# Kernel tuning notes

Measured on AMD Instinct MI355X. Metric: run time of the kernel, lower is better.

## Reference

```python
import jax, jax.numpy as jnp
import numpy as np

B, S, D_MODEL, D_EMB, H = 2, 2048, 1024, 1024, 16
D_K = D_EMB // H


def setup_inputs() -> dict:
    key = jax.random.key(0)
    ks = jax.random.split(key, 14)
    sd_in = 1.0 / np.sqrt(D_MODEL)
    sd_e = 1.0 / np.sqrt(D_EMB)
    inp = {
        'q': jax.random.normal(ks[0], (B, S, D_MODEL), jnp.float32),
        'k': jax.random.normal(ks[1], (B, S, D_MODEL), jnp.float32),
        'v': jax.random.normal(ks[2], (B, S, D_MODEL), jnp.float32),
        # causal mask: 1 = attend, 0 = blocked (built from ones via tril)
        'mask': jnp.tril(jnp.ones((S, S), jnp.int32))[None].repeat(B, axis=0),
        # weights stored [in, out] (equivalent to torch Linear weight.T)
        'W_in': jax.random.uniform(ks[3], (D_MODEL, D_EMB), jnp.float32, -sd_in, sd_in),
        'b_in': jax.random.uniform(ks[4], (D_EMB,), jnp.float32, -sd_in, sd_in),
        'Wq': jax.random.uniform(ks[5], (D_EMB, D_EMB), jnp.float32, -sd_e, sd_e),
        'bq': jax.random.uniform(ks[6], (D_EMB,), jnp.float32, -sd_e, sd_e),
        'Wk': jax.random.uniform(ks[7], (D_EMB, D_EMB), jnp.float32, -sd_e, sd_e),
        'bk': jax.random.uniform(ks[8], (D_EMB,), jnp.float32, -sd_e, sd_e),
        'Wv': jax.random.uniform(ks[9], (D_EMB, D_EMB), jnp.float32, -sd_e, sd_e),
        'bv': jax.random.uniform(ks[10], (D_EMB,), jnp.float32, -sd_e, sd_e),
        'Wo': jax.random.uniform(ks[11], (D_EMB, D_MODEL), jnp.float32, -sd_e, sd_e),
        'bo': jax.random.uniform(ks[12], (D_MODEL,), jnp.float32, -sd_e, sd_e),
    }
    return inp


def reference(q, k, v, mask, W_in, b_in, Wq, bq, Wk, bk, Wv, bv, Wo, bo):
    bs = q.shape[0]
    # shared input projection applied to q, k, v (as in the torch module)
    q_p = q @ W_in + b_in
    k_p = k @ W_in + b_in
    v_p = v @ W_in + b_in
    # per-head projections -> [B, H, S, d_k]
    def heads(x):
        return x.reshape(bs, -1, H, D_K).transpose(0, 2, 1, 3)
    qh = heads(q_p @ Wq + bq)
    kh = heads(k_p @ Wk + bk)
    vh = heads(v_p @ Wv + bv)
    scores = jnp.einsum('bhqd,bhkd->bhqk', qh, kh) / np.sqrt(D_K).astype(np.float32)
    scores = jnp.where(mask[:, None, :, :] == 0, jnp.float32(-1e9), scores)
    attn = jax.nn.softmax(scores, axis=-1)  # dropout in eval mode = identity
    out_h = jnp.einsum('bhqk,bhkd->bhqd', attn, vh)
    concat = out_h.transpose(0, 2, 1, 3).reshape(bs, -1, D_EMB)
    return concat @ Wo + bo
```

## Files before the change

### kernel.cpp

```cpp
#include <hip/hip_runtime.h>
#include <hip/hip_bf16.h>
#include <stdint.h>

typedef __bf16 bf16;
typedef __bf16 bf16x4 __attribute__((ext_vector_type(4)));
typedef __bf16 bf16x8 __attribute__((ext_vector_type(8)));
typedef float  f32x4 __attribute__((ext_vector_type(4)));

#define MFMA16(a,b,c) __builtin_amdgcn_mfma_f32_16x16x32_bf16((a),(b),(c),0,0,0)

__device__ __forceinline__ void gld_lds16(const void* g, void* lds_base) {
  __builtin_amdgcn_global_load_lds(
      (const __attribute__((address_space(1))) unsigned int*)g,
      (__attribute__((address_space(3))) unsigned int*)(unsigned int)(uintptr_t)lds_base,
      16, 0, 0);
}

struct Cast4 { const float* src[4]; bf16* dst[4]; int nblk[4]; };
__global__ __launch_bounds__(256) void cast_bf16_k4(Cast4 c) {
  const int z = blockIdx.y;
  if ((int)blockIdx.x >= c.nblk[z]) return;
  const float* __restrict__ x = c.src[z];
  bf16* __restrict__ y = c.dst[z];
  size_t i = ((size_t)blockIdx.x * 256 + threadIdx.x) * 8;
  float4 a = *(const float4*)(x + i);
  float4 b = *(const float4*)(x + i + 4);
  bf16x8 o;
  o[0] = (bf16)a.x; o[1] = (bf16)a.y; o[2] = (bf16)a.z; o[3] = (bf16)a.w;
  o[4] = (bf16)b.x; o[5] = (bf16)b.y; o[6] = (bf16)b.z; o[7] = (bf16)b.w;
  *(bf16x8*)(y + i) = o;
}

struct TC4 { const float* src[4]; bf16* dst[4]; };
__global__ __launch_bounds__(256) void transpose_cast4(TC4 t) {
  __shared__ float tile[32][33];
  const float* __restrict__ W = t.src[blockIdx.z];
  bf16* __restrict__ Wt = t.dst[blockIdx.z];
  const int kbase = blockIdx.y * 32, nbase = blockIdx.x * 32;
  const int tx = threadIdx.x & 31, ty = threadIdx.x >> 5;
#pragma unroll
  for (int i = 0; i < 4; ++i)
    tile[ty + 8 * i][tx] = W[(size_t)(kbase + ty + 8 * i) * 1024 + nbase + tx];
  __syncthreads();
#pragma unroll
  for (int i = 0; i < 4; ++i)
    Wt[(size_t)(nbase + ty + 8 * i) * 1024 + kbase + tx] = (bf16)tile[tx][ty + 8 * i];
}

__global__ __launch_bounds__(256) void bias_combine(
    const float* __restrict__ b_in,
    const float* __restrict__ W0, const float* __restrict__ W1, const float* __restrict__ W2,
    const float* __restrict__ a0, const float* __restrict__ a1, const float* __restrict__ a2,
    float* __restrict__ outbase) {
  __shared__ float red[4][64];
  const int z = blockIdx.y;
  const float* W = z == 0 ? W0 : (z == 1 ? W1 : W2);
  const float* ba = z == 0 ? a0 : (z == 1 ? a1 : a2);
  const int tj = threadIdx.x & 63, ti = threadIdx.x >> 6;
  const int j = blockIdx.x * 64 + tj;
  float s = 0.f;
#pragma unroll 16
  for (int i = ti * 256; i < ti * 256 + 256; ++i) s += b_in[i] * W[(size_t)i * 1024 + j];
  red[ti][tj] = s;
  __syncthreads();
  if (ti == 0)
    outbase[z * 1024 + j] = ba[j] + red[0][tj] + red[1][tj] + red[2][tj] + red[3][tj];
}

struct Gemm3 {
  const bf16* A[3];
  const bf16* Bt[3];
  const float* bias[3];
  void* C[3];
  int vtz;
  bf16* Cvt;
};

template <bool OUT_BF16, int BN>
__global__ __launch_bounds__(256) void gemm_bt(Gemm3 g, int M, int N, int K) {
  constexpr int NB = BN / 32;
  const int nx = N / BN, nyl = (M >> 7) >> 3;
  const int bx = blockIdx.x;
  const int xcd = bx & 7;
  const int ib = bx >> 3;
  const int z = ib / (nx * nyl);
  const int r = ib - z * (nx * nyl);
  const int x = r / nyl;
  const int yl = r - x * nyl;
  const int y = xcd * nyl + yl;

  const bf16* __restrict__ A  = g.A[z];
  const bf16* __restrict__ Bt = g.Bt[z];
  const float* bias = g.bias[z];
  void* C = g.C[z];

  __shared__ bf16 As[128 * 64];
  __shared__ bf16 Bs[BN * 64];

  const int tid = threadIdx.x;
  const int lane = tid & 63;
  const int w = tid >> 6;
  const int wr = w >> 1, wc = w & 1;
  const int l16 = lane & 15, kg = lane >> 4;
  const int m0 = y * 128, n0 = x * BN;

  f32x4 acc[4][NB] = {};

  for (int k0 = 0; k0 < K; k0 += 64) {
#pragma unroll
    for (int i = 0; i < 4; ++i) {
      const int gc = i * 256 + tid;
      const int row = gc >> 3, ch = gc & 7;
      const int lch = ch ^ (row & 7);
      gld_lds16(A + (size_t)(m0 + row) * K + k0 + lch * 8,
                (char*)As + i * 4096 + w * 1024);
    }
#pragma unroll
    for (int i = 0; i < NB; ++i) {
      const int gc = i * 256 + tid;
      const int row = gc >> 3, ch = gc & 7;
      const int lch = ch ^ (row & 7);
      gld_lds16(Bt + (size_t)(n0 + row) * K + k0 + lch * 8,
                (char*)Bs + i * 4096 + w * 1024);
    }
    __syncthreads();
#pragma unroll
    for (int kk = 0; kk < 2; ++kk) {
      const int cc = kk * 4 + kg;
      bf16x8 af[4], bfr[NB];
#pragma unroll
      for (int m = 0; m < 4; ++m) {
        const int rr = wr * 64 + m * 16 + l16;
        af[m] = *(const bf16x8*)((const char*)As + rr * 128 + ((cc ^ (rr & 7)) << 4));
      }
#pragma unroll
      for (int n = 0; n < NB; ++n) {
        const int rn = wc * (BN / 2) + n * 16 + l16;
        bfr[n] = *(const bf16x8*)((const char*)Bs + rn * 128 + ((cc ^ (rn & 7)) << 4));
      }
#pragma unroll
      for (int m = 0; m < 4; ++m)
#pragma unroll
        for (int n = 0; n < NB; ++n)
          acc[m][n] = MFMA16(af[m], bfr[n], acc[m][n]);
    }
    __syncthreads();
  }

  if (z == g.vtz) {
#pragma unroll
    for (int m = 0; m < 4; ++m) {
      const int row0 = m0 + wr * 64 + m * 16 + kg * 4;
#pragma unroll
      for (int n = 0; n < NB; ++n) {
        const int col = n0 + wc * (BN / 2) + n * 16 + l16;
        const float bb = bias ? bias[col] : 0.f;
        bf16x4 pk;
#pragma unroll
        for (int i = 0; i < 4; ++i) pk[i] = (bf16)(acc[m][n][i] + bb);
        *(bf16x4*)(g.Cvt + (size_t)col * M + row0) = pk;
      }
    }
    return;
  }

#pragma unroll
  for (int m = 0; m < 4; ++m) {
    const int row0 = m0 + wr * 64 + m * 16 + kg * 4;
#pragma unroll
    for (int n = 0; n < NB; ++n) {
      const int col = n0 + wc * (BN / 2) + n * 16 + l16;
      const float bb = bias ? bias[col] : 0.f;
#pragma unroll
      for (int i = 0; i < 4; ++i) {
        float val = acc[m][n][i] + bb;
        if (OUT_BF16) ((bf16*)C)[(size_t)(row0 + i) * N + col] = (bf16)val;
        else          ((float*)C)[(size_t)(row0 + i) * N + col] = val;
      }
    }
  }
}

#define SEQL 2048
__global__ __launch_bounds__(512) void attn_flash(const bf16* __restrict__ qh,
                                                  const bf16* __restrict__ kh,
                                                  const bf16* __restrict__ vt,
                                                  bf16* __restrict__ conc) {
  const int bx = blockIdx.x;
  const int xcd = bx & 7, j = bx >> 3;
  const int half = j >> 5, jj = j & 31;
  const int bh = xcd * 4 + (jj >> 3);
  const int tq = jj & 7;
  const int rb = half ? tq : 15 - tq;
  const int b = bh >> 4, h = bh & 15;
  const int tid = threadIdx.x, lane = tid & 63, w = tid >> 6;
  const int wh = w >> 2;
  const int l16 = lane & 15, kg = lane >> 4;

  __shared__ bf16 KsB[2 * 8192];
  __shared__ bf16 VsB[2 * 8192];
  __shared__ bf16 Ps[8 * 1024];

  char* Psw = (char*)Ps + w * 2048;
  const size_t kvbase = ((size_t)(b * SEQL)) * 1024 + h * 64;
  const bf16* vbase = vt + ((size_t)(h * 64)) * 4096 + b * SEQL;

  auto stage = [&](int buf, int p) {
    const int j0 = p * 128;
#pragma unroll
    for (int c = 0; c < 2; ++c) {
      const int idx = c * 512 + tid;
      const int kr = idx >> 3;
      const int kch = (idx & 7) ^ (kr & 7);
      gld_lds16(kh + kvbase + (size_t)(j0 + kr) * 1024 + kch * 8,
                (char*)KsB + buf * 16384 + c * 8192 + w * 1024);
      const int vr = idx >> 4;
      const int vch = (idx & 15) ^ (vr & 15);
      gld_lds16(vbase + (size_t)vr * 4096 + j0 + vch * 8,
                (char*)VsB + buf * 16384 + c * 8192 + w * 1024);
    }
  };

  bf16x8 onesv;
#pragma unroll
  for (int i = 0; i < 8; ++i) onesv[i] = (bf16)1.0f;

  const int q0a = rb * 128;
  const int npairs = rb + 1;
  const int myrow0 = q0a + wh * 64 + (w & 3) * 16;
  const int rowmax = q0a + wh * 64 + 63;

  const int qrow = myrow0 + l16;
  const size_t qoff = ((size_t)(b * SEQL) + qrow) * 1024 + h * 64;
  const bf16x8 qf0 = *(const bf16x8*)(qh + qoff + kg * 8);
  const bf16x8 qf1 = *(const bf16x8*)(qh + qoff + 32 + kg * 8);

  f32x4 acc[4] = {};
  f32x4 accl = {};
  constexpr float SCL = 0.18033688011112042f;

  stage(0, 0);
  __syncthreads();

  for (int p = 0; p < npairs; ++p) {
    const int cur = p & 1;
    if (p + 1 < npairs) stage(cur ^ 1, p + 1);

    const char* Kb = (const char*)KsB + cur * 16384;
    const char* Vb = (const char*)VsB + cur * 16384;

#pragma unroll
    for (int s = 0; s < 2; ++s) {
      const int j0 = p * 128 + s * 64;
      if (j0 > rowmax) continue;

      f32x4 sc[4];
      __builtin_amdgcn_s_setprio(1);
#pragma unroll
      for (int kb = 0; kb < 4; ++kb) {
        const int r = s * 64 + kb * 16 + l16;
        bf16x8 kf0 = *(const bf16x8*)(Kb + r * 128 + ((kg ^ (r & 7)) << 4));
        bf16x8 kf1 = *(const bf16x8*)(Kb + r * 128 + (((4 + kg) ^ (r & 7)) << 4));
        f32x4 cfr = {};
        cfr = MFMA16(qf0, kf0, cfr);
        sc[kb] = MFMA16(qf1, kf1, cfr);
      }
      __builtin_amdgcn_s_setprio(0);

      if (j0 + 63 > myrow0) {
#pragma unroll
        for (int kb = 0; kb < 4; ++kb) {
          const int key = j0 + kb * 16 + l16;
#pragma unroll
          for (int i = 0; i < 4; ++i) {
            const int row = myrow0 + kg * 4 + i;
            if (key > row) sc[kb][i] = -1e9f;
          }
        }
      }
#pragma unroll
      for (int kb = 0; kb < 4; ++kb)
#pragma unroll
        for (int i = 0; i < 4; ++i) {
          const float pp2 = __builtin_exp2f(sc[kb][i] * SCL);
          const int prr = kg * 4 + i;
          const int ce = kb * 16 + l16;
          *(bf16*)(Psw + prr * 128 + ((((ce >> 3) ^ (prr & 7)) << 4) | ((ce & 7) * 2))) =
              (bf16)pp2;
        }

      __builtin_amdgcn_s_setprio(1);
#pragma unroll
      for (int kc = 0; kc < 2; ++kc) {
        bf16x8 pf = *(const bf16x8*)(Psw + l16 * 128 + ((((kc * 4 + kg) ^ (l16 & 7)) << 4)));
        accl = MFMA16(pf, onesv, accl);
#pragma unroll
        for (int nb = 0; nb < 4; ++nb) {
          const int rr = nb * 16 + l16;
          const int c16 = s * 8 + kc * 4 + kg;
          bf16x8 vf = *(const bf16x8*)(Vb + rr * 256 + ((c16 ^ (rr & 15)) << 4));
          acc[nb] = MFMA16(pf, vf, acc[nb]);
        }
      }
      __builtin_amdgcn_s_setprio(0);
    }
    __syncthreads();
  }

#pragma unroll
  for (int nb = 0; nb < 4; ++nb)
#pragma unroll
    for (int i = 0; i < 4; ++i) {
      const float val = acc[nb][i] / accl[i];
      const int row = myrow0 + kg * 4 + i;
      conc[((size_t)(b * SEQL) + row) * 1024 + h * 64 + nb * 16 + l16] = (bf16)val;
    }
}

extern "C" void kernel_launch(void* const* d_in, const int* in_sizes, int n_in,
                              void* d_out, int out_size, void* d_ws, size_t ws_size,
                              hipStream_t stream) {
  (void)in_sizes; (void)n_in; (void)out_size; (void)ws_size;
  const float* q    = (const float*)d_in[0];
  const float* k    = (const float*)d_in[1];
  const float* v    = (const float*)d_in[2];
  const float* W_in = (const float*)d_in[4];
  const float* b_in = (const float*)d_in[5];
  const float* Wq = (const float*)d_in[6];  const float* bq = (const float*)d_in[7];
  const float* Wk = (const float*)d_in[8];  const float* bk = (const float*)d_in[9];
  const float* Wv = (const float*)d_in[10]; const float* bv = (const float*)d_in[11];
  const float* Wo = (const float*)d_in[12]; const float* bo = (const float*)d_in[13];

  const size_t SA = (size_t)4096 * 1024;
  const size_t SW = (size_t)1024 * 1024;
  bf16* p = (bf16*)d_ws;
  bf16* qb  = p; p += SA;
  bf16* kb  = p; p += SA;
  bf16* vb  = p; p += SA;
  bf16* qhb = p; p += SA;
  bf16* khb = p; p += SA;
  bf16* vhb = p; p += SA;
  bf16* Wib = p; p += SW;
  bf16* Wtq = p; p += SW;
  bf16* Wtk = p; p += SW;
  bf16* Wtv = p; p += SW;
  bf16* Wto = p; p += SW;
  bf16* Wc0 = p; p += SW;
  bf16* Wc1 = p; p += SW;
  bf16* Wc2 = p; p += SW;
  float* bc = (float*)p;
  bf16* conc = qb;
  bf16* vtb = Wib;

  Cast4 cc;
  cc.src[0] = q;  cc.dst[0] = qb;  cc.nblk[0] = 2048;
  cc.src[1] = k;  cc.dst[1] = kb;  cc.nblk[1] = 2048;
  cc.src[2] = v;  cc.dst[2] = vb;  cc.nblk[2] = 2048;
  cc.src[3] = W_in; cc.dst[3] = Wib; cc.nblk[3] = 512;
  cast_bf16_k4<<<dim3(2048, 4), 256, 0, stream>>>(cc);

  TC4 tc;
  tc.src[0] = Wq; tc.dst[0] = Wtq;
  tc.src[1] = Wk; tc.dst[1] = Wtk;
  tc.src[2] = Wv; tc.dst[2] = Wtv;
  tc.src[3] = Wo; tc.dst[3] = Wto;
  transpose_cast4<<<dim3(32, 32, 4), 256, 0, stream>>>(tc);

  bias_combine<<<dim3(16, 3), 256, 0, stream>>>(b_in, Wq, Wk, Wv, bq, bk, bv, bc);

  Gemm3 gc;
  gc.A[0] = Wtq; gc.A[1] = Wtk; gc.A[2] = Wtv;
  gc.Bt[0] = Wib; gc.Bt[1] = Wib; gc.Bt[2] = Wib;
  gc.bias[0] = nullptr; gc.bias[1] = nullptr; gc.bias[2] = nullptr;
  gc.C[0] = Wc0; gc.C[1] = Wc1; gc.C[2] = Wc2;
  gc.vtz = -1; gc.Cvt = nullptr;
  gemm_bt<true, 64><<<dim3(384), 256, 0, stream>>>(gc, 1024, 1024, 1024);

  Gemm3 gp;
  gp.A[0] = qb; gp.A[1] = kb; gp.A[2] = vb;
  gp.Bt[0] = Wc0; gp.Bt[1] = Wc1; gp.Bt[2] = Wc2;
  gp.bias[0] = bc; gp.bias[1] = bc + 1024; gp.bias[2] = bc + 2048;
  gp.C[0] = qhb; gp.C[1] = khb; gp.C[2] = vhb;
  gp.vtz = 2; gp.Cvt = vtb;
  gemm_bt<true, 128><<<dim3(768), 256, 0, stream>>>(gp, 4096, 1024, 1024);

  attn_flash<<<dim3(512), 512, 0, stream>>>(qhb, khb, vtb, conc);

  Gemm3 gf;
  gf.A[0] = conc; gf.A[1] = conc; gf.A[2] = conc;
  gf.Bt[0] = Wto; gf.Bt[1] = Wto; gf.Bt[2] = Wto;
  gf.bias[0] = bo; gf.bias[1] = bo; gf.bias[2] = bo;
  gf.C[0] = d_out; gf.C[1] = d_out; gf.C[2] = d_out;
  gf.vtz = -1; gf.Cvt = nullptr;
  gemm_bt<false, 64><<<dim3(512), 256, 0, stream>>>(gf, 4096, 1024, 1024);
}
```

Baseline: 139.3 us.

## Fuse fp32-to-bf16 activation cast into projection GEMM A-tile loads

Result: no change. 138.5 us (-0.6%).

```diff
diff --git a/kernel.cpp b/kernel.cpp
--- a/kernel.cpp
+++ b/kernel.cpp
@@ -16,12 +16,8 @@
       16, 0, 0);
 }
 
-struct Cast4 { const float* src[4]; bf16* dst[4]; int nblk[4]; };
-__global__ __launch_bounds__(256) void cast_bf16_k4(Cast4 c) {
-  const int z = blockIdx.y;
-  if ((int)blockIdx.x >= c.nblk[z]) return;
-  const float* __restrict__ x = c.src[z];
-  bf16* __restrict__ y = c.dst[z];
+__global__ __launch_bounds__(256) void cast_bf16_k(const float* __restrict__ x,
+                                                   bf16* __restrict__ y) {
   size_t i = ((size_t)blockIdx.x * 256 + threadIdx.x) * 8;
   float4 a = *(const float4*)(x + i);
   float4 b = *(const float4*)(x + i + 4);
@@ -68,7 +64,7 @@
 }
 
 struct Gemm3 {
-  const bf16* A[3];
+  const void* A[3];
   const bf16* Bt[3];
   const float* bias[3];
   void* C[3];
@@ -76,7 +72,7 @@
   bf16* Cvt;
 };
 
-template <bool OUT_BF16, int BN>
+template <bool OUT_BF16, int BN, bool CVTA>
 __global__ __launch_bounds__(256) void gemm_bt(Gemm3 g, int M, int N, int K) {
   constexpr int NB = BN / 32;
   const int nx = N / BN, nyl = (M >> 7) >> 3;
@@ -89,7 +85,8 @@
   const int yl = r - x * nyl;
   const int y = xcd * nyl + yl;
 
-  const bf16* __restrict__ A  = g.A[z];
+  const bf16* __restrict__ Ab  = CVTA ? nullptr : (const bf16*)g.A[z];
+  const float* __restrict__ Af = CVTA ? (const float*)g.A[z] : nullptr;
   const bf16* __restrict__ Bt = g.Bt[z];
   const float* bias = g.bias[z];
   void* C = g.C[z];
@@ -106,14 +103,47 @@
 
   f32x4 acc[4][NB] = {};
 
-  for (int k0 = 0; k0 < K; k0 += 64) {
+  float4 av[4][2];
+  auto loadA = [&](int k0) {
+#pragma unroll
+    for (int i = 0; i < 4; ++i) {
+      const int gc = i * 256 + tid;
+      const int row = gc >> 3, ch = gc & 7;
+      const float* s = Af + (size_t)(m0 + row) * K + k0 + ch * 8;
+      av[i][0] = *(const float4*)s;
+      av[i][1] = *(const float4*)(s + 4);
+    }
+  };
+  auto writeA = [&]() {
 #pragma unroll
     for (int i = 0; i < 4; ++i) {
       const int gc = i * 256 + tid;
       const int row = gc >> 3, ch = gc & 7;
       const int lch = ch ^ (row & 7);
-      gld_lds16(A + (size_t)(m0 + row) * K + k0 + lch * 8,
-                (char*)As + i * 4096 + w * 1024);
+      bf16x8 o;
+      o[0] = (bf16)av[i][0].x; o[1] = (bf16)av[i][0].y;
+      o[2] = (bf16)av[i][0].z; o[3] = (bf16)av[i][0].w;
+      o[4] = (bf16)av[i][1].x; o[5] = (bf16)av[i][1].y;
+      o[6] = (bf16)av[i][1].z; o[7] = (bf16)av[i][1].w;
+      *(bf16x8*)((char*)As + row * 128 + lch * 16) = o;
+    }
+  };
+
+  if (CVTA) loadA(0);
+
+  for (int k0 = 0; k0 < K; k0 += 64) {
+    if (CVTA) {
+      writeA();
+      if (k0 + 64 < K) loadA(k0 + 64);
+    } else {
+#pragma unroll
+      for (int i = 0; i < 4; ++i) {
+        const int gc = i * 256 + tid;
+        const int row = gc >> 3, ch = gc & 7;
+        const int lch = ch ^ (row & 7);
+        gld_lds16(Ab + (size_t)(m0 + row) * K + k0 + lch * 8,
+                  (char*)As + i * 4096 + w * 1024);
+      }
     }
 #pragma unroll
     for (int i = 0; i < NB; ++i) {
@@ -352,12 +382,7 @@
   bf16* conc = qb;
   bf16* vtb = Wib;
 
-  Cast4 cc;
-  cc.src[0] = q;  cc.dst[0] = qb;  cc.nblk[0] = 2048;
-  cc.src[1] = k;  cc.dst[1] = kb;  cc.nblk[1] = 2048;
-  cc.src[2] = v;  cc.dst[2] = vb;  cc.nblk[2] = 2048;
-  cc.src[3] = W_in; cc.dst[3] = Wib; cc.nblk[3] = 512;
-  cast_bf16_k4<<<dim3(2048, 4), 256, 0, stream>>>(cc);
+  cast_bf16_k<<<dim3(512), 256, 0, stream>>>(W_in, Wib);
 
   TC4 tc;
   tc.src[0] = Wq; tc.dst[0] = Wtq;
@@ -374,15 +399,15 @@
   gc.bias[0] = nullptr; gc.bias[1] = nullptr; gc.bias[2] = nullptr;
   gc.C[0] = Wc0; gc.C[1] = Wc1; gc.C[2] = Wc2;
   gc.vtz = -1; gc.Cvt = nullptr;
-  gemm_bt<true, 64><<<dim3(384), 256, 0, stream>>>(gc, 1024, 1024, 1024);
+  gemm_bt<true, 64, false><<<dim3(384), 256, 0, stream>>>(gc, 1024, 1024, 1024);
 
   Gemm3 gp;
-  gp.A[0] = qb; gp.A[1] = kb; gp.A[2] = vb;
+  gp.A[0] = q; gp.A[1] = k; gp.A[2] = v;
   gp.Bt[0] = Wc0; gp.Bt[1] = Wc1; gp.Bt[2] = Wc2;
   gp.bias[0] = bc; gp.bias[1] = bc + 1024; gp.bias[2] = bc + 2048;
   gp.C[0] = qhb; gp.C[1] = khb; gp.C[2] = vhb;
   gp.vtz = 2; gp.Cvt = vtb;
-  gemm_bt<true, 128><<<dim3(768), 256, 0, stream>>>(gp, 4096, 1024, 1024);
+  gemm_bt<true, 128, true><<<dim3(768), 256, 0, stream>>>(gp, 4096, 1024, 1024);
 
   attn_flash<<<dim3(512), 512, 0, stream>>>(qhb, khb, vtb, conc);
 
@@ -392,5 +417,5 @@
   gf.bias[0] = bo; gf.bias[1] = bo; gf.bias[2] = bo;
   gf.C[0] = d_out; gf.C[1] = d_out; gf.C[2] = d_out;
   gf.vtz = -1; gf.Cvt = nullptr;
-  gemm_bt<false, 64><<<dim3(512), 256, 0, stream>>>(gf, 4096, 1024, 1024);
-}
+  gemm_bt<false, 64, false><<<dim3(512), 256, 0, stream>>>(gf, 4096, 1024, 1024);
+}
```

## Merge prep kernels and overlap q/k/v casting with weight-combine GEMM

Applied to the files above, without the earlier changes.

New measurement: 127.8 us, median of 2. 1.09x faster.

```diff
diff --git a/kernel.cpp b/kernel.cpp
--- a/kernel.cpp
+++ b/kernel.cpp
@@ -16,55 +16,54 @@
       16, 0, 0);
 }
 
-struct Cast4 { const float* src[4]; bf16* dst[4]; int nblk[4]; };
-__global__ __launch_bounds__(256) void cast_bf16_k4(Cast4 c) {
-  const int z = blockIdx.y;
-  if ((int)blockIdx.x >= c.nblk[z]) return;
-  const float* __restrict__ x = c.src[z];
-  bf16* __restrict__ y = c.dst[z];
-  size_t i = ((size_t)blockIdx.x * 256 + threadIdx.x) * 8;
-  float4 a = *(const float4*)(x + i);
-  float4 b = *(const float4*)(x + i + 4);
-  bf16x8 o;
-  o[0] = (bf16)a.x; o[1] = (bf16)a.y; o[2] = (bf16)a.z; o[3] = (bf16)a.w;
-  o[4] = (bf16)b.x; o[5] = (bf16)b.y; o[6] = (bf16)b.z; o[7] = (bf16)b.w;
-  *(bf16x8*)(y + i) = o;
-}
-
-struct TC4 { const float* src[4]; bf16* dst[4]; };
-__global__ __launch_bounds__(256) void transpose_cast4(TC4 t) {
+struct PrepArgs {
+  const float* W_in; bf16* Wib;
+  const float* Wsrc[4]; bf16* Wdst[4];
+  const float* b_in;
+  const float* Wz[3]; const float* bz[3];
+  float* bc;
+};
+__global__ __launch_bounds__(256) void prep_all(PrepArgs a) {
   __shared__ float tile[32][33];
-  const float* __restrict__ W = t.src[blockIdx.z];
-  bf16* __restrict__ Wt = t.dst[blockIdx.z];
-  const int kbase = blockIdx.y * 32, nbase = blockIdx.x * 32;
-  const int tx = threadIdx.x & 31, ty = threadIdx.x >> 5;
-#pragma unroll
-  for (int i = 0; i < 4; ++i)
-    tile[ty + 8 * i][tx] = W[(size_t)(kbase + ty + 8 * i) * 1024 + nbase + tx];
-  __syncthreads();
-#pragma unroll
-  for (int i = 0; i < 4; ++i)
-    Wt[(size_t)(nbase + ty + 8 * i) * 1024 + kbase + tx] = (bf16)tile[tx][ty + 8 * i];
-}
-
-__global__ __launch_bounds__(256) void bias_combine(
-    const float* __restrict__ b_in,
-    const float* __restrict__ W0, const float* __restrict__ W1, const float* __restrict__ W2,
-    const float* __restrict__ a0, const float* __restrict__ a1, const float* __restrict__ a2,
-    float* __restrict__ outbase) {
   __shared__ float red[4][64];
-  const int z = blockIdx.y;
-  const float* W = z == 0 ? W0 : (z == 1 ? W1 : W2);
-  const float* ba = z == 0 ? a0 : (z == 1 ? a1 : a2);
-  const int tj = threadIdx.x & 63, ti = threadIdx.x >> 6;
-  const int j = blockIdx.x * 64 + tj;
-  float s = 0.f;
+  const int bx = blockIdx.x, tid = threadIdx.x;
+  if (bx < 512) {
+    size_t i = ((size_t)bx * 256 + tid) * 8;
+    float4 x = *(const float4*)(a.W_in + i);
+    float4 y = *(const float4*)(a.W_in + i + 4);
+    bf16x8 o;
+    o[0] = (bf16)x.x; o[1] = (bf16)x.y; o[2] = (bf16)x.z; o[3] = (bf16)x.w;
+    o[4] = (bf16)y.x; o[5] = (bf16)y.y; o[6] = (bf16)y.z; o[7] = (bf16)y.w;
+    *(bf16x8*)(a.Wib + i) = o;
+  } else if (bx < 4608) {
+    const int idx = bx - 512;
+    const int wz = idx >> 10, rem = idx & 1023;
+    const int kbase = (rem >> 5) * 32, nbase = (rem & 31) * 32;
+    const float* __restrict__ W = a.Wsrc[wz];
+    bf16* __restrict__ Wt = a.Wdst[wz];
+    const int tx = tid & 31, ty = tid >> 5;
+#pragma unroll
+    for (int i = 0; i < 4; ++i)
+      tile[ty + 8 * i][tx] = W[(size_t)(kbase + ty + 8 * i) * 1024 + nbase + tx];
+    __syncthreads();
+#pragma unroll
+    for (int i = 0; i < 4; ++i)
+      Wt[(size_t)(nbase + ty + 8 * i) * 1024 + kbase + tx] = (bf16)tile[tx][ty + 8 * i];
+  } else {
+    const int idx = bx - 4608;
+    const int z = idx >> 4, jb = idx & 15;
+    const float* W = a.Wz[z];
+    const float* ba = a.bz[z];
+    const int tj = tid & 63, ti = tid >> 6;
+    const int j = jb * 64 + tj;
+    float s = 0.f;
 #pragma unroll 16
-  for (int i = ti * 256; i < ti * 256 + 256; ++i) s += b_in[i] * W[(size_t)i * 1024 + j];
-  red[ti][tj] = s;
-  __syncthreads();
-  if (ti == 0)
-    outbase[z * 1024 + j] = ba[j] + red[0][tj] + red[1][tj] + red[2][tj] + red[3][tj];
+    for (int i = ti * 256; i < ti * 256 + 256; ++i) s += a.b_in[i] * W[(size_t)i * 1024 + j];
+    red[ti][tj] = s;
+    __syncthreads();
+    if (ti == 0)
+      a.bc[z * 1024 + j] = ba[j] + red[0][tj] + red[1][tj] + red[2][tj] + red[3][tj];
+  }
 }
 
 struct Gemm3 {
@@ -77,10 +76,9 @@
 };
 
 template <bool OUT_BF16, int BN>
-__global__ __launch_bounds__(256) void gemm_bt(Gemm3 g, int M, int N, int K) {
+__device__ __forceinline__ void gemm_core(const Gemm3& g, int M, int N, int K, int bx) {
   constexpr int NB = BN / 32;
   const int nx = N / BN, nyl = (M >> 7) >> 3;
-  const int bx = blockIdx.x;
   const int xcd = bx & 7;
   const int ib = bx >> 3;
   const int z = ib / (nx * nyl);
@@ -177,6 +175,34 @@
         if (OUT_BF16) ((bf16*)C)[(size_t)(row0 + i) * N + col] = (bf16)val;
         else          ((float*)C)[(size_t)(row0 + i) * N + col] = val;
       }
+    }
+  }
+}
+
+template <bool OUT_BF16, int BN>
+__global__ __launch_bounds__(256) void gemm_bt(Gemm3 g, int M, int N, int K) {
+  gemm_core<OUT_BF16, BN>(g, M, N, K, blockIdx.x);
+}
+
+struct CastQKV { const float* src[3]; bf16* dst[3]; };
+__global__ __launch_bounds__(256) void combine_cast(Gemm3 g, CastQKV c) {
+  if ((int)blockIdx.x < 384) {
+    gemm_core<true, 64>(g, 1024, 1024, 1024, blockIdx.x);
+  } else {
+    const int cb = blockIdx.x - 384;
+#pragma unroll
+    for (int it = 0; it < 12; ++it) {
+      const int chunk = (it * 512 + cb) * 256 + (int)threadIdx.x;
+      const int arr = chunk >> 19;
+      const size_t off = (size_t)(chunk & 524287) << 3;
+      const float* __restrict__ s = c.src[arr];
+      bf16* __restrict__ d = c.dst[arr];
+      float4 x = *(const float4*)(s + off);
+      float4 y = *(const float4*)(s + off + 4);
+      bf16x8 o;
+      o[0] = (bf16)x.x; o[1] = (bf16)x.y; o[2] = (bf16)x.z; o[3] = (bf16)x.w;
+      o[4] = (bf16)y.x; o[5] = (bf16)y.y; o[6] = (bf16)y.z; o[7] = (bf16)y.w;
+      *(bf16x8*)(d + off) = o;
     }
   }
 }
@@ -352,21 +378,17 @@
   bf16* conc = qb;
   bf16* vtb = Wib;
 
-  Cast4 cc;
-  cc.src[0] = q;  cc.dst[0] = qb;  cc.nblk[0] = 2048;
-  cc.src[1] = k;  cc.dst[1] = kb;  cc.nblk[1] = 2048;
-  cc.src[2] = v;  cc.dst[2] = vb;  cc.nblk[2] = 2048;
-  cc.src[3] = W_in; cc.dst[3] = Wib; cc.nblk[3] = 512;
-  cast_bf16_k4<<<dim3(2048, 4), 256, 0, stream>>>(cc);
-
-  TC4 tc;
-  tc.src[0] = Wq; tc.dst[0] = Wtq;
-  tc.src[1] = Wk; tc.dst[1] = Wtk;
-  tc.src[2] = Wv; tc.dst[2] = Wtv;
-  tc.src[3] = Wo; tc.dst[3] = Wto;
-  transpose_cast4<<<dim3(32, 32, 4), 256, 0, stream>>>(tc);
-
-  bias_combine<<<dim3(16, 3), 256, 0, stream>>>(b_in, Wq, Wk, Wv, bq, bk, bv, bc);
+  PrepArgs pa;
+  pa.W_in = W_in; pa.Wib = Wib;
+  pa.Wsrc[0] = Wq; pa.Wdst[0] = Wtq;
+  pa.Wsrc[1] = Wk; pa.Wdst[1] = Wtk;
+  pa.Wsrc[2] = Wv; pa.Wdst[2] = Wtv;
+  pa.Wsrc[3] = Wo; pa.Wdst[3] = Wto;
+  pa.b_in = b_in;
+  pa.Wz[0] = Wq; pa.Wz[1] = Wk; pa.Wz[2] = Wv;
+  pa.bz[0] = bq; pa.bz[1] = bk; pa.bz[2] = bv;
+  pa.bc = bc;
+  prep_all<<<dim3(4656), 256, 0, stream>>>(pa);
 
   Gemm3 gc;
   gc.A[0] = Wtq; gc.A[1] = Wtk; gc.A[2] = Wtv;
@@ -374,7 +396,10 @@
   gc.bias[0] = nullptr; gc.bias[1] = nullptr; gc.bias[2] = nullptr;
   gc.C[0] = Wc0; gc.C[1] = Wc1; gc.C[2] = Wc2;
   gc.vtz = -1; gc.Cvt = nullptr;
-  gemm_bt<true, 64><<<dim3(384), 256, 0, stream>>>(gc, 1024, 1024, 1024);
+  CastQKV cq;
+  cq.src[0] = q; cq.src[1] = k; cq.src[2] = v;
+  cq.dst[0] = qb; cq.dst[1] = kb; cq.dst[2] = vb;
+  combine_cast<<<dim3(896), 256, 0, stream>>>(gc, cq);
 
   Gemm3 gp;
   gp.A[0] = qb; gp.A[1] = kb; gp.A[2] = vb;
```
